# Optimization experiments

Measured on AMD Instinct MI355X. Metric: run time of the kernel, lower is better.

## Reference

```python
import jax, jax.numpy as jnp
import numpy as np

HEAD_SIZE = 128
N_EMBED = 2048
B, T = 4, 4096


def setup_inputs() -> dict:
    key = jax.random.key(0)
    kx, kq, kk, kv = jax.random.split(key, 4)
    s = 1.0 / np.sqrt(N_EMBED)
    return {
        "x": jax.random.normal(kx, (B, T, N_EMBED), dtype=jnp.float32),
        "Wq": jax.random.normal(kq, (N_EMBED, HEAD_SIZE), dtype=jnp.float32) * s,
        "Wk": jax.random.normal(kk, (N_EMBED, HEAD_SIZE), dtype=jnp.float32) * s,
        "Wv": jax.random.normal(kv, (N_EMBED, HEAD_SIZE), dtype=jnp.float32) * s,
    }


def reference(x, Wq, Wk, Wv):
    # x: [B, T, C]; projections (no bias)
    q = jnp.einsum('btc,cd->btd', x, Wq)  # [B, T, D]
    k = jnp.einsum('btc,cd->btd', x, Wk)
    v = jnp.einsum('btc,cd->btd', x, Wv)
    scale = q.shape[-1] ** -0.5
    scores = jnp.einsum('btd,bsd->bts', q, k) * scale  # [B, T, T]
    T_ = x.shape[1]
    causal = jnp.tril(jnp.ones((T_, T_), dtype=bool))
    scores = jnp.where(causal, scores, -jnp.inf)
    weight = jax.nn.softmax(scores, axis=-1)
    # dropout is identity in eval mode
    out = jnp.einsum('bts,bsd->btd', weight, v)  # [B, T, D]
    return out
```

## Files before the change

### kernel.cpp

```cpp
#include <hip/hip_runtime.h>
#include <hip/hip_bf16.h>
#include <stdint.h>

typedef unsigned short ushort_t;
typedef short v8s __attribute__((ext_vector_type(8)));
typedef float f32x4 __attribute__((ext_vector_type(4)));
typedef float f32x16 __attribute__((ext_vector_type(16)));

#define MFMA16(a, b, c) __builtin_amdgcn_mfma_f32_16x16x32_bf16(a, b, c, 0, 0, 0)
#define MFMA32(a, b, c) __builtin_amdgcn_mfma_f32_32x32x16_bf16(a, b, c, 0, 0, 0)

typedef __attribute__((address_space(1))) void gvoid;
typedef __attribute__((address_space(3))) void svoid;

__device__ __forceinline__ void gld16(const void* g, void* s) {
    __builtin_amdgcn_global_load_lds((gvoid*)g, (svoid*)s, 16, 0, 0);
}

__device__ __forceinline__ ushort_t f2bf(float f) {
    union { __hip_bfloat16 b; ushort_t u; } c;
    c.b = __float2bfloat16(f);
    return c.u;
}

__device__ __forceinline__ unsigned f2bf2(float a, float b) {
    union { __hip_bfloat162 b2; unsigned u; } c;
    c.b2 = __float22bfloat162_rn(make_float2(a, b));
    return c.u;
}

__global__ void transpose_w(const float* __restrict__ Wq, const float* __restrict__ Wk,
                            const float* __restrict__ Wv, ushort_t* __restrict__ WT) {
    __shared__ float tile[64][132];
    int bid = blockIdx.x;
    int w = bid >> 5;
    int k0 = (bid & 31) << 6;
    const float* W = (w == 0) ? Wq : ((w == 1) ? Wk : Wv);
    int tid = threadIdx.x;
    #pragma unroll
    for (int i = 0; i < 8; i++) {
        int row = i * 8 + (tid >> 5);
        int col = (tid & 31) * 4;
        float4 v = *(const float4*)(W + (size_t)(k0 + row) * 128 + col);
        tile[row][col] = v.x; tile[row][col + 1] = v.y;
        tile[row][col + 2] = v.z; tile[row][col + 3] = v.w;
    }
    __syncthreads();
    int n = tid >> 1, kh = (tid & 1) * 32;
    ushort_t* dst = WT + ((size_t)(w * 128 + n)) * 2048 + k0 + kh;
    #pragma unroll
    for (int j = 0; j < 32; j += 4) {
        union { ushort_t u[4]; uint2 v2; } pk;
        #pragma unroll
        for (int e = 0; e < 4; e++) pk.u[e] = f2bf(tile[kh + j + e][n]);
        *(uint2*)(dst + j) = pk.v2;
    }
}

#define PJ_CVT_WRITE(RS, PAR)                                                 \
    {                                                                         \
        union { unsigned u[4]; v8s v; } p0, p1;                               \
        p0.u[0] = f2bf2(RS[0][0], RS[0][1]); p0.u[1] = f2bf2(RS[0][2], RS[0][3]); \
        p0.u[2] = f2bf2(RS[1][0], RS[1][1]); p0.u[3] = f2bf2(RS[1][2], RS[1][3]); \
        p1.u[0] = f2bf2(RS[2][0], RS[2][1]); p1.u[1] = f2bf2(RS[2][2], RS[2][3]); \
        p1.u[2] = f2bf2(RS[3][0], RS[3][1]); p1.u[3] = f2bf2(RS[3][2], RS[3][3]); \
        *(v8s*)((char*)abuf + (PAR) * 8192 + awb0) = p0.v;                    \
        *(v8s*)((char*)abuf + (PAR) * 8192 + awb1) = p1.v;                    \
    }

#define PJ_STEP(PAR, J, RLOAD, RCVT, DOX, DOB)                                \
    {                                                                         \
        if (DOB) {                                                            \
            int itn = (koff + (J) + 1) & 31;                                  \
            _Pragma("unroll")                                                 \
            for (int i = 0; i < 4; i++)                                       \
                gld16(bsrc[i] + (size_t)itn * 128,                            \
                      (char*)bbuf + ((PAR) ^ 1) * 16384 + (4 * wid + i) * 1024); \
        }                                                                     \
        __builtin_amdgcn_sched_barrier(0);                                    \
        if (DOX) {                                                            \
            int itx = (koff + (J) + 2) & 31;                                  \
            _Pragma("unroll")                                                 \
            for (int c = 0; c < 4; c++)                                       \
                RLOAD[c] = *(const f32x4*)(xp + (size_t)itx * 256 + c * 16);  \
        }                                                                     \
        __builtin_amdgcn_sched_barrier(0);                                    \
        const char* ab = (const char*)abuf + (PAR) * 8192;                    \
        const char* bb = (const char*)bbuf + (PAR) * 16384;                   \
        _Pragma("unroll")                                                     \
        for (int kk = 0; kk < 2; kk++) {                                      \
            v8s af[2], bf[4];                                                 \
            _Pragma("unroll")                                                 \
            for (int m = 0; m < 2; m++) {                                     \
                int row = wr * 32 + m * 16 + lr;                              \
                af[m] = *(const v8s*)(ab + row * 128 +                        \
                         ((kk * 64 + lg * 16) ^ ((row & 7) << 4)));           \
            }                                                                 \
            _Pragma("unroll")                                                 \
            for (int n = 0; n < 4; n++) {                                     \
                int row = wc * 64 + n * 16 + lr;                              \
                bf[n] = *(const v8s*)(bb + row * 128 +                        \
                         ((kk * 64 + lg * 16) ^ ((row & 7) << 4)));           \
            }                                                                 \
            __builtin_amdgcn_s_setprio(1);                                    \
            _Pragma("unroll")                                                 \
            for (int m = 0; m < 2; m++)                                       \
                _Pragma("unroll")                                             \
                for (int n = 0; n < 4; n++)                                   \
                    acc[m][n] = MFMA16(af[m], bf[n], acc[m][n]);              \
            __builtin_amdgcn_s_setprio(0);                                    \
        }                                                                     \
        if (DOB) {                                                            \
            PJ_CVT_WRITE(RCVT, (PAR) ^ 1);                                    \
            if (DOX) { asm volatile("s_waitcnt vmcnt(4)" ::: "memory"); }     \
            else     { asm volatile("s_waitcnt vmcnt(0)" ::: "memory"); }     \
            asm volatile("s_waitcnt lgkmcnt(0)" ::: "memory");                \
            __builtin_amdgcn_s_barrier();                                     \
        }                                                                     \
    }

__launch_bounds__(256, 3)
__global__ void proj_kernel(const float* __restrict__ x, const ushort_t* __restrict__ WT,
                            ushort_t* __restrict__ q, ushort_t* __restrict__ kb,
                            ushort_t* __restrict__ vb) {
    __shared__ ushort_t abuf[2][4096];
    __shared__ ushort_t bbuf[2][8192];

    int bid = blockIdx.x;
    int xcd = bid & 7, idx = bid >> 3;
    int mt_local = idx / 3, ng = idx - 3 * mt_local;
    int mtile = xcd * 32 + mt_local;
    size_t m0 = (size_t)mtile * 64;
    int c0 = ng * 128;
    int koff = ((bid >> 8) * 11) & 31;
    int tid = threadIdx.x, lane = tid & 63, wid = tid >> 6;
    int lg = lane >> 4, lr = lane & 15;
    int wr = wid >> 1, wc = wid & 1;

    f32x4 acc[2][4];
    #pragma unroll
    for (int m = 0; m < 2; m++)
        #pragma unroll
        for (int n = 0; n < 4; n++) acc[m][n] = (f32x4){0.f, 0.f, 0.f, 0.f};

    int ar = 16 * wid + (lane >> 2);
    const char* xp = (const char*)x + (m0 + ar) * 8192 + (lane & 3) * 64;
    int aswz = (ar & 7) << 4;
    int awb0 = ar * 128 + (((lane & 3) * 32 + 0) ^ aswz);
    int awb1 = ar * 128 + (((lane & 3) * 32 + 16) ^ aswz);

    const char* bsrc[4];
    #pragma unroll
    for (int i = 0; i < 4; i++) {
        int row = 8 * (4 * wid + i) + (lane >> 3);
        int col = ((lane & 7) * 16) ^ ((row & 7) << 4);
        bsrc[i] = (const char*)WT + (size_t)(c0 + row) * 4096 + col;
    }

    f32x4 xs0[4], xs1[4];
    {
        int it0 = koff, it1 = (koff + 1) & 31;
        #pragma unroll
        for (int i = 0; i < 4; i++)
            gld16(bsrc[i] + (size_t)it0 * 128, (char*)bbuf + (4 * wid + i) * 1024);
        #pragma unroll
        for (int c = 0; c < 4; c++) xs0[c] = *(const f32x4*)(xp + (size_t)it0 * 256 + c * 16);
        #pragma unroll
        for (int c = 0; c < 4; c++) xs1[c] = *(const f32x4*)(xp + (size_t)it1 * 256 + c * 16);
        PJ_CVT_WRITE(xs0, 0);
        asm volatile("s_waitcnt vmcnt(0)" ::: "memory");
        asm volatile("s_waitcnt lgkmcnt(0)" ::: "memory");
        __builtin_amdgcn_s_barrier();
    }

    for (int j = 0; j < 30; j += 2) {
        PJ_STEP(0, j,     xs0, xs1, 1, 1);
        PJ_STEP(1, j + 1, xs1, xs0, 1, 1);
    }
    PJ_STEP(0, 30, xs0, xs1, 0, 1);
    PJ_STEP(1, 31, xs1, xs0, 0, 0);

    #pragma unroll
    for (int m = 0; m < 2; m++) {
        #pragma unroll
        for (int e = 0; e < 4; e++) {
            size_t row = m0 + (size_t)(wr * 32 + m * 16 + 4 * lg + e);
            int t = (int)(row & 4095);
            size_t base = (row >> 12) * 524288;
            #pragma unroll
            for (int n = 0; n < 4; n++) {
                int d = (wc * 64 + n * 16 + lr) & 127;
                ushort_t val = f2bf(acc[m][n][e]);
                if (ng == 0)
                    q[base + (size_t)(t >> 5) * 4096 + (d >> 4) * 512 + ((d >> 3) & 1) * 256 + (t & 31) * 8 + (d & 7)] = val;
                else if (ng == 1)
                    kb[base + (size_t)(t >> 5) * 4096 + (d >> 4) * 512 + ((d >> 3) & 1) * 256 + (t & 31) * 8 + (d & 7)] = val;
                else
                    vb[base + (size_t)(t >> 4) * 2048 + (d >> 5) * 512 + ((t >> 3) & 1) * 256 + (d & 31) * 8 + (t & 7)] = val;
            }
        }
    }
}

__device__ __forceinline__ f32x16 zero16() {
    f32x16 z;
    #pragma unroll
    for (int i = 0; i < 16; i++) z[i] = 0.f;
    return z;
}

#define ATT_PVC(SV, BASE, VC, CNEXT)                                          \
    {                                                                         \
        unsigned a0 = f2bf2(SV[(BASE) + 0], SV[(BASE) + 1]);                  \
        unsigned a1 = f2bf2(SV[(BASE) + 2], SV[(BASE) + 3]);                  \
        unsigned b0 = f2bf2(SV[(BASE) + 4], SV[(BASE) + 5]);                  \
        unsigned b1 = f2bf2(SV[(BASE) + 6], SV[(BASE) + 7]);                  \
        unsigned snd0 = hi ? a0 : b0, snd1 = hi ? a1 : b1;                    \
        unsigned rcv0 = (unsigned)__shfl_xor((int)snd0, 32);                  \
        unsigned rcv1 = (unsigned)__shfl_xor((int)snd1, 32);                  \
        union { unsigned u[4]; v8s v; } pf;                                   \
        pf.u[0] = hi ? rcv0 : a0;                                             \
        pf.u[1] = hi ? rcv1 : a1;                                             \
        pf.u[2] = hi ? b0 : rcv0;                                             \
        pf.u[3] = hi ? b1 : rcv1;                                             \
        __builtin_amdgcn_s_setprio(1);                                        \
        _Pragma("unroll")                                                     \
        for (int dt = 0; dt < 4; dt++)                                        \
            accO[dt] = MFMA32(VC[dt], pf.v, accO[dt]);                        \
        __builtin_amdgcn_s_setprio(0);                                        \
        if ((CNEXT) >= 0) {                                                   \
            _Pragma("unroll")                                                 \
            for (int dt = 0; dt < 4; dt++)                                    \
                VC[dt] = *(const v8s*)(vg + (CNEXT) * 2048 + dt * 512);       \
        }                                                                     \
    }

__launch_bounds__(256, 2)
__global__ void attn_kernel(const ushort_t* __restrict__ q, const ushort_t* __restrict__ kb,
                            const ushort_t* __restrict__ vb, float* __restrict__ out) {
    __shared__ float obuf[4][4][16][64];
    __shared__ float stat[2][4][64];

    int bid = blockIdx.x;
    int xcd = bid & 7, rk = bid >> 3;
    int b = xcd >> 1;
    int g = rk * 2 + (xcd & 1);
    int qt = (g & 1) ? (g >> 1) : (127 - (g >> 1));
    int qt0 = qt * 32;
    int tid = threadIdx.x, lane = tid & 63, wid = tid >> 6;
    int hi = lane >> 5, lo = lane & 31;
    size_t bb = (size_t)b * 524288;
    int nt = (qt >> 1) + 1;
    const float cexp = 0.08838834764831845f * 1.4426950408889634f;

    v8s qf[8];
    {
        const ushort_t* qg = q + bb + (size_t)qt * 4096 + (size_t)lane * 8;
        #pragma unroll
        for (int ks = 0; ks < 8; ks++) qf[ks] = *(const v8s*)(qg + ks * 512);
    }

    f32x16 accO[4];
    #pragma unroll
    for (int dt = 0; dt < 4; dt++) accO[dt] = zero16();
    float mrun = -1e30f, lrun = 0.f;

    for (int t = wid; t < nt; t += 4) {
        const ushort_t* kg = kb + bb + (size_t)t * 8192 + (size_t)lane * 8;
        const ushort_t* vg = vb + bb + (size_t)t * 8192 + (size_t)lane * 8;

        f32x16 s0 = zero16(), s1 = zero16();
        __builtin_amdgcn_s_setprio(1);
        #pragma unroll
        for (int ks = 0; ks < 8; ks++) {
            v8s kf = *(const v8s*)(kg + ks * 512);
            s0 = MFMA32(kf, qf[ks], s0);
        }
        #pragma unroll
        for (int ks = 0; ks < 8; ks++) {
            v8s kf = *(const v8s*)(kg + 4096 + ks * 512);
            s1 = MFMA32(kf, qf[ks], s1);
        }
        __builtin_amdgcn_s_setprio(0);

        v8s vA[4], vB[4];
        #pragma unroll
        for (int dt = 0; dt < 4; dt++) vA[dt] = *(const v8s*)(vg + dt * 512);
        #pragma unroll
        for (int dt = 0; dt < 4; dt++) vB[dt] = *(const v8s*)(vg + 2048 + dt * 512);

        if (t == nt - 1) {
            int qrow = qt0 + lo;
            #pragma unroll
            for (int r = 0; r < 16; r++) {
                int kvb = t * 64 + (r & 3) + 8 * (r >> 2) + 4 * hi;
                if (kvb > qrow) s0[r] = -1e30f;
                if (kvb + 32 > qrow) s1[r] = -1e30f;
            }
        }

        float mx = s0[0];
        #pragma unroll
        for (int r = 1; r < 16; r++) mx = fmaxf(mx, s0[r]);
        #pragma unroll
        for (int r = 0; r < 16; r++) mx = fmaxf(mx, s1[r]);
        mx = fmaxf(mx, __shfl_xor(mx, 32));

        if (__any(mx > mrun + 62.7f)) {
            float mnew = fmaxf(mrun, mx);
            float fr = exp2f((mrun - mnew) * cexp);
            lrun *= fr;
            #pragma unroll
            for (int dt = 0; dt < 4; dt++)
                #pragma unroll
                for (int r = 0; r < 16; r++) accO[dt][r] *= fr;
            mrun = mnew;
        }
        float mc = mrun * cexp;
        float rs = 0.f;
        #pragma unroll
        for (int r = 0; r < 16; r++) { s0[r] = exp2f(fmaf(s0[r], cexp, -mc)); rs += s0[r]; }
        #pragma unroll
        for (int r = 0; r < 16; r++) { s1[r] = exp2f(fmaf(s1[r], cexp, -mc)); rs += s1[r]; }
        rs += __shfl_xor(rs, 32);
        lrun += rs;

        ATT_PVC(s0, 0, vA, 2);
        ATT_PVC(s0, 8, vB, 3);
        ATT_PVC(s1, 0, vA, -1);
        ATT_PVC(s1, 8, vB, -1);
    }

    #pragma unroll
    for (int dt = 0; dt < 4; dt++)
        #pragma unroll
        for (int r = 0; r < 16; r++)
            obuf[wid][dt][r][lane] = accO[dt][r];
    stat[0][wid][lane] = mrun;
    stat[1][wid][lane] = lrun;
    __syncthreads();

    float m0 = stat[0][0][lane], m1 = stat[0][1][lane];
    float m2 = stat[0][2][lane], m3 = stat[0][3][lane];
    float m = fmaxf(fmaxf(m0, m1), fmaxf(m2, m3));
    float f0 = exp2f((m0 - m) * cexp), f1 = exp2f((m1 - m) * cexp);
    float f2 = exp2f((m2 - m) * cexp), f3 = exp2f((m3 - m) * cexp);
    float lsum = f0 * stat[1][0][lane] + f1 * stat[1][1][lane]
               + f2 * stat[1][2][lane] + f3 * stat[1][3][lane];
    float linv = 1.0f / lsum;

    float o[16];
    #pragma unroll
    for (int r = 0; r < 16; r++)
        o[r] = (f0 * obuf[0][wid][r][lane] + f1 * obuf[1][wid][r][lane]
              + f2 * obuf[2][wid][r][lane] + f3 * obuf[3][wid][r][lane]) * linv;

    float* orow = out + ((size_t)b * 4096 + qt0 + lo) * 128 + wid * 32 + 4 * hi;
    #pragma unroll
    for (int a = 0; a < 4; a++) {
        float4 vv;
        vv.x = o[4 * a + 0]; vv.y = o[4 * a + 1];
        vv.z = o[4 * a + 2]; vv.w = o[4 * a + 3];
        *(float4*)(orow + 8 * a) = vv;
    }
}

extern "C" void kernel_launch(void* const* d_in, const int* in_sizes, int n_in,
                              void* d_out, int out_size, void* d_ws, size_t ws_size,
                              hipStream_t stream) {
    const float* x  = (const float*)d_in[0];
    const float* Wq = (const float*)d_in[1];
    const float* Wk = (const float*)d_in[2];
    const float* Wv = (const float*)d_in[3];
    float* out = (float*)d_out;
    char* ws = (char*)d_ws;

    ushort_t* q  = (ushort_t*)(ws);
    ushort_t* kb = (ushort_t*)(ws + (4u << 20));
    ushort_t* vb = (ushort_t*)(ws + (8u << 20));
    ushort_t* WT = (ushort_t*)(ws + (12u << 20));

    transpose_w<<<dim3(96), dim3(256), 0, stream>>>(Wq, Wk, Wv, WT);
    proj_kernel<<<dim3(768), dim3(256), 0, stream>>>(x, WT, q, kb, vb);
    attn_kernel<<<dim3(512), dim3(256), 0, stream>>>(q, kb, vb, out);
}
```

Measured before the change: 104.4 us.

## Coalesce x loads across lanes and drop staggered K start offset

Each x-tile load now has 16 consecutive lanes read one contiguous 256-byte row segment, instead of each lane reading 64 contiguous bytes spread over four rows. LDS writes become four 8-byte stores per lane with a matching swizzle. The per-block rotated K start (koff) is removed, so all blocks walk K from zero and the modulo indexing goes away. This is meant to improve global load coalescing for the fp32 activation stream, at the risk of more blocks hitting the same weight and x columns at once.

```diff
diff --git a/kernel.cpp b/kernel.cpp
--- a/kernel.cpp
+++ b/kernel.cpp
@@ -57,33 +57,34 @@
     }
 }
 
+#define PJ_XLOAD(S, IT)                                                       \
+    {                                                                         \
+        _Pragma("unroll")                                                     \
+        for (int i = 0; i < 4; i++)                                           \
+            S[i] = *(const f32x4*)(xsrc[i] + (size_t)(IT) * 256);             \
+    }
+
 #define PJ_CVT_WRITE(RS, PAR)                                                 \
     {                                                                         \
-        union { unsigned u[4]; v8s v; } p0, p1;                               \
-        p0.u[0] = f2bf2(RS[0][0], RS[0][1]); p0.u[1] = f2bf2(RS[0][2], RS[0][3]); \
-        p0.u[2] = f2bf2(RS[1][0], RS[1][1]); p0.u[3] = f2bf2(RS[1][2], RS[1][3]); \
-        p1.u[0] = f2bf2(RS[2][0], RS[2][1]); p1.u[1] = f2bf2(RS[2][2], RS[2][3]); \
-        p1.u[2] = f2bf2(RS[3][0], RS[3][1]); p1.u[3] = f2bf2(RS[3][2], RS[3][3]); \
-        *(v8s*)((char*)abuf + (PAR) * 8192 + awb0) = p0.v;                    \
-        *(v8s*)((char*)abuf + (PAR) * 8192 + awb1) = p1.v;                    \
-    }
-
-#define PJ_STEP(PAR, J, RLOAD, RCVT, DOX, DOB)                                \
+        _Pragma("unroll")                                                     \
+        for (int i = 0; i < 4; i++) {                                         \
+            uint2 p;                                                          \
+            p.x = f2bf2(RS[i][0], RS[i][1]);                                  \
+            p.y = f2bf2(RS[i][2], RS[i][3]);                                  \
+            *(uint2*)((char*)abuf + (PAR) * 8192 + awb[i]) = p;               \
+        }                                                                     \
+    }
+
+#define PJ_STEP(PAR, IT, RLOAD, RCVT, DOX, DOB)                               \
     {                                                                         \
         if (DOB) {                                                            \
-            int itn = (koff + (J) + 1) & 31;                                  \
             _Pragma("unroll")                                                 \
             for (int i = 0; i < 4; i++)                                       \
-                gld16(bsrc[i] + (size_t)itn * 128,                            \
+                gld16(bsrc[i] + (size_t)((IT) + 1) * 128,                     \
                       (char*)bbuf + ((PAR) ^ 1) * 16384 + (4 * wid + i) * 1024); \
         }                                                                     \
         __builtin_amdgcn_sched_barrier(0);                                    \
-        if (DOX) {                                                            \
-            int itx = (koff + (J) + 2) & 31;                                  \
-            _Pragma("unroll")                                                 \
-            for (int c = 0; c < 4; c++)                                       \
-                RLOAD[c] = *(const f32x4*)(xp + (size_t)itx * 256 + c * 16);  \
-        }                                                                     \
+        if (DOX) PJ_XLOAD(RLOAD, (IT) + 2);                                   \
         __builtin_amdgcn_sched_barrier(0);                                    \
         const char* ab = (const char*)abuf + (PAR) * 8192;                    \
         const char* bb = (const char*)bbuf + (PAR) * 16384;                   \
@@ -132,7 +133,6 @@
     int mtile = xcd * 32 + mt_local;
     size_t m0 = (size_t)mtile * 64;
     int c0 = ng * 128;
-    int koff = ((bid >> 8) * 11) & 31;
     int tid = threadIdx.x, lane = tid & 63, wid = tid >> 6;
     int lg = lane >> 4, lr = lane & 15;
     int wr = wid >> 1, wc = wid & 1;
@@ -143,11 +143,14 @@
         #pragma unroll
         for (int n = 0; n < 4; n++) acc[m][n] = (f32x4){0.f, 0.f, 0.f, 0.f};
 
-    int ar = 16 * wid + (lane >> 2);
-    const char* xp = (const char*)x + (m0 + ar) * 8192 + (lane & 3) * 64;
-    int aswz = (ar & 7) << 4;
-    int awb0 = ar * 128 + (((lane & 3) * 32 + 0) ^ aswz);
-    int awb1 = ar * 128 + (((lane & 3) * 32 + 16) ^ aswz);
+    const char* xsrc[4];
+    int awb[4];
+    #pragma unroll
+    for (int i = 0; i < 4; i++) {
+        int row = 16 * wid + 4 * i + (lane >> 4);
+        xsrc[i] = (const char*)x + (m0 + row) * 8192 + (lane & 15) * 16;
+        awb[i] = row * 128 + (((lane & 15) * 8) ^ ((row & 7) << 4));
+    }
 
     const char* bsrc[4];
     #pragma unroll
@@ -158,24 +161,19 @@
     }
 
     f32x4 xs0[4], xs1[4];
-    {
-        int it0 = koff, it1 = (koff + 1) & 31;
-        #pragma unroll
-        for (int i = 0; i < 4; i++)
-            gld16(bsrc[i] + (size_t)it0 * 128, (char*)bbuf + (4 * wid + i) * 1024);
-        #pragma unroll
-        for (int c = 0; c < 4; c++) xs0[c] = *(const f32x4*)(xp + (size_t)it0 * 256 + c * 16);
-        #pragma unroll
-        for (int c = 0; c < 4; c++) xs1[c] = *(const f32x4*)(xp + (size_t)it1 * 256 + c * 16);
-        PJ_CVT_WRITE(xs0, 0);
-        asm volatile("s_waitcnt vmcnt(0)" ::: "memory");
-        asm volatile("s_waitcnt lgkmcnt(0)" ::: "memory");
-        __builtin_amdgcn_s_barrier();
-    }
-
-    for (int j = 0; j < 30; j += 2) {
-        PJ_STEP(0, j,     xs0, xs1, 1, 1);
-        PJ_STEP(1, j + 1, xs1, xs0, 1, 1);
+    #pragma unroll
+    for (int i = 0; i < 4; i++)
+        gld16(bsrc[i], (char*)bbuf + (4 * wid + i) * 1024);
+    PJ_XLOAD(xs0, 0);
+    PJ_XLOAD(xs1, 1);
+    PJ_CVT_WRITE(xs0, 0);
+    asm volatile("s_waitcnt vmcnt(0)" ::: "memory");
+    asm volatile("s_waitcnt lgkmcnt(0)" ::: "memory");
+    __builtin_amdgcn_s_barrier();
+
+    for (int it = 0; it < 30; it += 2) {
+        PJ_STEP(0, it,     xs0, xs1, 1, 1);
+        PJ_STEP(1, it + 1, xs1, xs0, 1, 1);
     }
     PJ_STEP(0, 30, xs0, xs1, 0, 1);
     PJ_STEP(1, 31, xs1, xs0, 0, 0);
```

New measurement: 98.08 us. 1.06x faster.
